# Optimization experiments

Hardware: AMD Instinct MI355X
Metric: run time of the kernel (lower is better)

Reference implementation:

```python
import jax, jax.numpy as jnp
import numpy as np

B, F, D, U = 4096, 32, 64, 256


def setup_inputs() -> dict:
    key = jax.random.key(0)
    k1, k2, k3, k4 = jax.random.split(key, 4)
    embeds = jax.random.normal(k1, (B, F, D), dtype=jnp.float32)
    # glorot-ish scaling for the learned weights
    linear_w = jax.random.normal(k2, (F * D, U), dtype=jnp.float32) * (2.0 / (F * D + U)) ** 0.5
    inner_w = jax.random.normal(k3, (U, F), dtype=jnp.float32) * (2.0 / (U + F)) ** 0.5
    outer_w = jax.random.normal(k4, (U, D, D), dtype=jnp.float32) * (2.0 / (2 * D)) ** 0.5
    return {"embeds": embeds, "linear_w": linear_w, "inner_w": inner_w, "outer_w": outer_w}


def reference(embeds, linear_w, inner_w, outer_w):
    b = embeds.shape[0]
    # linear signal lz: flatten fields and project -> [B, U]
    lz = embeds.reshape(b, -1) @ linear_w
    # inner products: per unit u, delta_u = sum_f w_{u,f} * e_f  -> [B, U, D];
    # lp_inner[b,u] = ||delta_u||^2 (collapses the per-unit TF loop into one einsum)
    delta = jnp.einsum('bfd,uf->bud', embeds, inner_w)
    lp_inner = jnp.sum(jnp.square(delta), axis=2)  # [B, U]
    # outer products: product = fs fs^T with fs = sum_f e_f; lp_outer[b,u] = <product_b, W_u>
    fs = jnp.sum(embeds, axis=1)  # [B, D]
    lp_outer = jnp.einsum('bi,bj,uij->bu', fs, fs, outer_w)  # [B, U]
    return jnp.concatenate([lz, lp_inner, lp_outer], axis=1)  # [B, 3U]
```

## Files before the change

kernel.cpp:

```cpp
#include <hip/hip_runtime.h>
#include <hip/hip_bf16.h>


#define KA 3072
#define KW 7168

typedef __attribute__((ext_vector_type(8))) short short8v;
typedef __attribute__((ext_vector_type(4))) float f32x4;

#define GLOAD(src, dst) __builtin_amdgcn_global_load_lds( \
    (const __attribute__((address_space(1))) void*)(src), \
    (__attribute__((address_space(3))) void*)(dst), 16, 0, 0)

static __device__ __forceinline__ short f2bf(float f) {
    union { float f; unsigned u; } v; v.f = f;
    unsigned r = v.u + 0x7fffu + ((v.u >> 16) & 1u);
    return (short)(r >> 16);
}
static __device__ __forceinline__ float bf2f(short s) {
    union { unsigned u; float f; } v; v.u = ((unsigned)(unsigned short)s) << 16;
    return v.f;
}
static __device__ __forceinline__ int cvtpk(float lo, float hi) {
    int r;
    asm("v_cvt_pk_bf16_f32 %0, %1, %2" : "=v"(r) : "v"(lo), "v"(hi));
    return r;
}

__global__ __launch_bounds__(256) void prep(const float* __restrict__ embeds,
                                            const float* __restrict__ lw,
                                            const float* __restrict__ iw,
                                            const float* __restrict__ ow,
                                            short* __restrict__ A,
                                            short* __restrict__ FS,
                                            short* __restrict__ Wt) {
    __shared__ float se[2048];
    __shared__ short sebf[2048];
    int t = threadIdx.x;

    if (blockIdx.x < 4096) {
        int b = blockIdx.x;
        const float* e = embeds + (size_t)b * 2048;
        short* arow = A + (size_t)b * KA;

        float4 v0 = ((const float4*)e)[t * 2];
        float4 v1 = ((const float4*)e)[t * 2 + 1];
        ((float4*)se)[t * 2] = v0;
        ((float4*)se)[t * 2 + 1] = v1;
        short8v sb;
        sb[0] = f2bf(v0.x); sb[1] = f2bf(v0.y); sb[2] = f2bf(v0.z); sb[3] = f2bf(v0.w);
        sb[4] = f2bf(v1.x); sb[5] = f2bf(v1.y); sb[6] = f2bf(v1.z); sb[7] = f2bf(v1.w);
        ((short8v*)sebf)[t] = sb;
        *(short8v*)&arow[t * 8] = sb;

        __syncthreads();
        if (t < 64) {
            float s = 0.f;
            #pragma unroll
            for (int f = 0; f < 32; ++f) s += se[f * 64 + t];
            FS[(size_t)b * 64 + t] = f2bf(s);
        }

        int wid = t >> 6, lane = t & 63;
        int tm = wid >> 1, tn = wid & 1;
        int lr = lane & 15, lk = (lane >> 4) * 8;
        f32x4 g = {0.f, 0.f, 0.f, 0.f};
        #pragma unroll
        for (int ks = 0; ks < 2; ++ks) {
            short8v a  = *(const short8v*)&sebf[(tm * 16 + lr) * 64 + ks * 32 + lk];
            short8v bb = *(const short8v*)&sebf[(tn * 16 + lr) * 64 + ks * 32 + lk];
            g = __builtin_amdgcn_mfma_f32_16x16x32_bf16(a, bb, g, 0, 0, 0);
        }
        #pragma unroll
        for (int r = 0; r < 4; ++r) {
            int grow = tm * 16 + (lane >> 4) * 4 + r;
            int gcol = tn * 16 + lr;
            arow[2048 + grow * 32 + gcol] = f2bf(g[r]);
        }
    } else {
        int u = blockIdx.x - 4096;
        short* w = Wt + (size_t)u * KW;

        for (int k = t; k < 2048; k += 256) w[k] = f2bf(lw[(size_t)k * 256 + u]);

        if (t < 32) se[t] = iw[u * 32 + t];
        __syncthreads();
        for (int idx = t; idx < 1024; idx += 256)
            w[2048 + idx] = f2bf(se[idx >> 5] * se[idx & 31]);

        const float* owu = ow + (size_t)u * 4096;
        for (int i = t; i < 512; i += 256) {
            float4 a = ((const float4*)owu)[i * 2];
            float4 b = ((const float4*)owu)[i * 2 + 1];
            short8v s;
            s[0] = f2bf(a.x); s[1] = f2bf(a.y); s[2] = f2bf(a.z); s[3] = f2bf(a.w);
            s[4] = f2bf(b.x); s[5] = f2bf(b.y); s[6] = f2bf(b.z); s[7] = f2bf(b.w);
            *(short8v*)&w[3072 + i * 8] = s;
        }
    }
}

__global__ __launch_bounds__(256) void gemm_tile(const short* __restrict__ A,
                                                 const short* __restrict__ Wt,
                                                 const short* __restrict__ FS,
                                                 float* __restrict__ out) {
    __shared__ short As[3][8192];
    __shared__ short Bs[3][4096];

    int id = blockIdx.x;
    int xcd = id & 7, slot = id >> 3, sgrp = slot >> 4, q = slot & 15;
    int seg = (sgrp == 0) ? 2 : (sgrp == 1) ? 0 : 1;
    int mt = xcd * 4 + (q >> 2), nt = q & 3;
    const int nk = (seg == 0) ? 32 : (seg == 1) ? 16 : 64;
    int brow = mt * 128, bcol = nt * 64;
    int akoff = (seg == 1) ? 2048 : 0;
    int boff  = (seg == 0) ? 0 : (seg == 1) ? 2048 : 3072;

    int t = threadIdx.x, w = t >> 6, lane = t & 63;
    int lr = lane & 15, hi = lane >> 4;
    int srow = t >> 3;
    int soct = (t & 7) ^ (srow & 7);

    const short* Asrc = A  + (size_t)(brow + srow) * KA + akoff + soct * 8;
    const short* Bsrc = Wt + (size_t)(bcol + srow) * KW + boff  + soct * 8;
    const short* Fsrc = FS + (size_t)(brow + srow) * 64 + soct * 8;

    auto stageA = [&](int p, int kt) {
        #pragma unroll
        for (int i = 0; i < 4; ++i)
            GLOAD(Asrc + (size_t)i * 32 * KA + kt * 64, &As[p][i * 2048 + t * 8]);
    };
    auto stageB = [&](int p, int kt) {
        #pragma unroll
        for (int i = 0; i < 2; ++i)
            GLOAD(Bsrc + (size_t)i * 32 * KW + kt * 64, &Bs[p][i * 2048 + t * 8]);
    };

    f32x4 acc[2][4];
    #pragma unroll
    for (int m = 0; m < 2; ++m)
        #pragma unroll
        for (int n = 0; n < 4; ++n) acc[m][n] = (f32x4){0.f, 0.f, 0.f, 0.f};

    auto compute = [&](const short* a_s, const short* b_s) {
        #pragma unroll
        for (int ks = 0; ks < 2; ++ks) {
            int oct = ((ks * 4 + hi) ^ (lr & 7)) * 8;
            short8v a[2], b[4];
            #pragma unroll
            for (int m = 0; m < 2; ++m)
                a[m] = *(const short8v*)&a_s[(w * 32 + m * 16 + lr) * 64 + oct];
            #pragma unroll
            for (int n = 0; n < 4; ++n)
                b[n] = *(const short8v*)&b_s[(n * 16 + lr) * 64 + oct];
            __builtin_amdgcn_s_setprio(1);
            #pragma unroll
            for (int m = 0; m < 2; ++m)
                #pragma unroll
                for (int n = 0; n < 4; ++n)
                    acc[m][n] = __builtin_amdgcn_mfma_f32_16x16x32_bf16(a[m], b[n], acc[m][n], 0, 0, 0);
            __builtin_amdgcn_s_setprio(0);
        }
    };

    if (seg != 2) {
        stageA(0, 0); stageB(0, 0);
        stageA(1, 1); stageB(1, 1);
        stageA(2, 2); stageB(2, 2);
        __builtin_amdgcn_sched_barrier(0);
        for (int kt = 0; kt < nk; ++kt) {
            int cur = kt % 3;
            if (kt + 2 < nk)      asm volatile("s_waitcnt vmcnt(12)" ::: "memory");
            else if (kt + 1 < nk) asm volatile("s_waitcnt vmcnt(6)" ::: "memory");
            else                  asm volatile("s_waitcnt vmcnt(0)" ::: "memory");
            __builtin_amdgcn_s_barrier();
            __builtin_amdgcn_sched_barrier(0);
            compute(As[cur], Bs[cur]);
            __builtin_amdgcn_sched_barrier(0);
            __builtin_amdgcn_s_barrier();
            if (kt + 3 < nk) { stageA(cur, kt + 3); stageB(cur, kt + 3); }
            __builtin_amdgcn_sched_barrier(0);
        }
    } else {
        #pragma unroll
        for (int i = 0; i < 4; ++i)
            GLOAD(Fsrc + (size_t)i * 32 * 64, &As[0][i * 2048 + t * 8]);
        stageB(0, 0); stageB(1, 1); stageB(2, 2);
        asm volatile("s_waitcnt vmcnt(6)" ::: "memory");
        __builtin_amdgcn_s_barrier();
        __builtin_amdgcn_sched_barrier(0);

        float fj[2][2][8];
        #pragma unroll
        for (int m = 0; m < 2; ++m)
            #pragma unroll
            for (int ks = 0; ks < 2; ++ks) {
                int oct = ((ks * 4 + hi) ^ (lr & 7)) * 8;
                short8v v = *(const short8v*)&As[0][(w * 32 + m * 16 + lr) * 64 + oct];
                #pragma unroll
                for (int e = 0; e < 8; ++e) fj[m][ks][e] = bf2f(v[e]);
            }
        for (int kt = 0; kt < 64; ++kt) {
            int cur = kt % 3;
            if (kt + 2 < 64)      asm volatile("s_waitcnt vmcnt(4)" ::: "memory");
            else if (kt + 1 < 64) asm volatile("s_waitcnt vmcnt(2)" ::: "memory");
            else                  asm volatile("s_waitcnt vmcnt(0)" ::: "memory");
            __builtin_amdgcn_s_barrier();
            __builtin_amdgcn_sched_barrier(0);
            int ioff = ((kt >> 3) ^ (lr & 7)) * 8 + (kt & 7);
            float s[2];
            #pragma unroll
            for (int m = 0; m < 2; ++m)
                s[m] = bf2f(As[0][(w * 32 + m * 16 + lr) * 64 + ioff]);
            #pragma unroll
            for (int ks = 0; ks < 2; ++ks) {
                int oct = ((ks * 4 + hi) ^ (lr & 7)) * 8;
                short8v b[4];
                #pragma unroll
                for (int n = 0; n < 4; ++n)
                    b[n] = *(const short8v*)&Bs[cur][(n * 16 + lr) * 64 + oct];
                #pragma unroll
                for (int m = 0; m < 2; ++m) {
                    union { int i32[4]; short8v v; } fa;
                    #pragma unroll
                    for (int q2 = 0; q2 < 4; ++q2)
                        fa.i32[q2] = cvtpk(s[m] * fj[m][ks][2 * q2], s[m] * fj[m][ks][2 * q2 + 1]);
                    __builtin_amdgcn_s_setprio(1);
                    #pragma unroll
                    for (int n = 0; n < 4; ++n)
                        acc[m][n] = __builtin_amdgcn_mfma_f32_16x16x32_bf16(fa.v, b[n], acc[m][n], 0, 0, 0);
                    __builtin_amdgcn_s_setprio(0);
                }
            }
            __builtin_amdgcn_sched_barrier(0);
            __builtin_amdgcn_s_barrier();
            if (kt + 3 < 64) stageB(cur, kt + 3);
            __builtin_amdgcn_sched_barrier(0);
        }
    }

    int segbase = seg * 256;
    #pragma unroll
    for (int m = 0; m < 2; ++m) {
        int row0 = brow + w * 32 + m * 16 + hi * 4;
        #pragma unroll
        for (int n = 0; n < 4; ++n) {
            int col = segbase + bcol + n * 16 + lr;
            #pragma unroll
            for (int r = 0; r < 4; ++r)
                out[(size_t)(row0 + r) * 768 + col] = acc[m][n][r];
        }
    }
}

extern "C" void kernel_launch(void* const* d_in, const int* in_sizes, int n_in,
                              void* d_out, int out_size, void* d_ws, size_t ws_size,
                              hipStream_t stream) {
    const float* embeds = (const float*)d_in[0];
    const float* lw = (const float*)d_in[1];
    const float* iw = (const float*)d_in[2];
    const float* ow = (const float*)d_in[3];
    float* out = (float*)d_out;

    short* A  = (short*)d_ws;
    short* Wt = A + (size_t)4096 * KA;
    short* FS = Wt + (size_t)256 * KW;

    prep<<<dim3(4352), dim3(256), 0, stream>>>(embeds, lw, iw, ow, A, FS, Wt);
    gemm_tile<<<dim3(384), dim3(256), 0, stream>>>(A, Wt, FS, out);
}
```

Baseline: 64.63 us.

## Split-K GEMM tiles into equal 16-step chunks with atomic accumulation

Work is split along K so every tile runs 16 k-steps: the linear segment is cut into 2 chunks and the outer segment into 4, and the grid grows from 384 to 896 blocks so the uneven per-segment load is balanced. Partial sums are combined with float atomic adds, so the prep kernel gets extra blocks that zero the output first. LDS pipelining drops from triple to double buffering, which frees shared memory and may raise occupancy. In exchange it adds atomic traffic, a zeroing pass, and a summation order that is no longer deterministic.

```diff
diff --git a/kernel.cpp b/kernel.cpp
--- a/kernel.cpp
+++ b/kernel.cpp
@@ -33,10 +33,19 @@
                                             const float* __restrict__ ow,
                                             short* __restrict__ A,
                                             short* __restrict__ FS,
-                                            short* __restrict__ Wt) {
+                                            short* __restrict__ Wt,
+                                            float4* __restrict__ outv) {
     __shared__ float se[2048];
     __shared__ short sebf[2048];
     int t = threadIdx.x;
+
+    if (blockIdx.x >= 4352) {
+        size_t i = (size_t)(blockIdx.x - 4352) * 256 + t;
+        #pragma unroll
+        for (int r = 0; r < 3; ++r)
+            outv[i + (size_t)r * 262144] = (float4){0.f, 0.f, 0.f, 0.f};
+        return;
+    }
 
     if (blockIdx.x < 4096) {
         int b = blockIdx.x;
@@ -104,17 +113,22 @@
                                                  const short* __restrict__ Wt,
                                                  const short* __restrict__ FS,
                                                  float* __restrict__ out) {
-    __shared__ short As[3][8192];
-    __shared__ short Bs[3][4096];
+    __shared__ short As[2][8192];
+    __shared__ short Bs[2][4096];
 
     int id = blockIdx.x;
-    int xcd = id & 7, slot = id >> 3, sgrp = slot >> 4, q = slot & 15;
-    int seg = (sgrp == 0) ? 2 : (sgrp == 1) ? 0 : 1;
-    int mt = xcd * 4 + (q >> 2), nt = q & 3;
-    const int nk = (seg == 0) ? 32 : (seg == 1) ? 16 : 64;
+    int xcd = id & 7, s = id >> 3;
+    int mtl = s & 3, part = s >> 2;
+    int ck = part >> 2, nt = part & 3;
+    int mt = xcd * 4 + mtl;
+    int seg, kc;
+    if (ck < 2)       { seg = 0; kc = ck; }
+    else if (ck == 2) { seg = 1; kc = 0; }
+    else              { seg = 2; kc = ck - 3; }
+    const int nk = 16;
     int brow = mt * 128, bcol = nt * 64;
-    int akoff = (seg == 1) ? 2048 : 0;
-    int boff  = (seg == 0) ? 0 : (seg == 1) ? 2048 : 3072;
+    int akoff = (seg == 0) ? kc * 1024 : 2048;
+    int boff  = (seg == 0) ? kc * 1024 : (seg == 1) ? 2048 : 3072 + kc * 1024;
 
     int t = threadIdx.x, w = t >> 6, lane = t & 63;
     int lr = lane & 15, hi = lane >> 4;
@@ -166,27 +180,25 @@
     if (seg != 2) {
         stageA(0, 0); stageB(0, 0);
         stageA(1, 1); stageB(1, 1);
-        stageA(2, 2); stageB(2, 2);
         __builtin_amdgcn_sched_barrier(0);
         for (int kt = 0; kt < nk; ++kt) {
-            int cur = kt % 3;
-            if (kt + 2 < nk)      asm volatile("s_waitcnt vmcnt(12)" ::: "memory");
-            else if (kt + 1 < nk) asm volatile("s_waitcnt vmcnt(6)" ::: "memory");
-            else                  asm volatile("s_waitcnt vmcnt(0)" ::: "memory");
+            int cur = kt & 1;
+            if (kt + 1 < nk) asm volatile("s_waitcnt vmcnt(6)" ::: "memory");
+            else             asm volatile("s_waitcnt vmcnt(0)" ::: "memory");
             __builtin_amdgcn_s_barrier();
             __builtin_amdgcn_sched_barrier(0);
             compute(As[cur], Bs[cur]);
             __builtin_amdgcn_sched_barrier(0);
             __builtin_amdgcn_s_barrier();
-            if (kt + 3 < nk) { stageA(cur, kt + 3); stageB(cur, kt + 3); }
+            if (kt + 2 < nk) { stageA(cur, kt + 2); stageB(cur, kt + 2); }
             __builtin_amdgcn_sched_barrier(0);
         }
     } else {
         #pragma unroll
         for (int i = 0; i < 4; ++i)
             GLOAD(Fsrc + (size_t)i * 32 * 64, &As[0][i * 2048 + t * 8]);
-        stageB(0, 0); stageB(1, 1); stageB(2, 2);
-        asm volatile("s_waitcnt vmcnt(6)" ::: "memory");
+        stageB(0, 0); stageB(1, 1);
+        asm volatile("s_waitcnt vmcnt(4)" ::: "memory");
         __builtin_amdgcn_s_barrier();
         __builtin_amdgcn_sched_barrier(0);
 
@@ -200,18 +212,18 @@
                 #pragma unroll
                 for (int e = 0; e < 8; ++e) fj[m][ks][e] = bf2f(v[e]);
             }
-        for (int kt = 0; kt < 64; ++kt) {
-            int cur = kt % 3;
-            if (kt + 2 < 64)      asm volatile("s_waitcnt vmcnt(4)" ::: "memory");
-            else if (kt + 1 < 64) asm volatile("s_waitcnt vmcnt(2)" ::: "memory");
-            else                  asm volatile("s_waitcnt vmcnt(0)" ::: "memory");
-            __builtin_amdgcn_s_barrier();
-            __builtin_amdgcn_sched_barrier(0);
-            int ioff = ((kt >> 3) ^ (lr & 7)) * 8 + (kt & 7);
-            float s[2];
+        for (int kt = 0; kt < nk; ++kt) {
+            int cur = kt & 1;
+            if (kt + 1 < nk) asm volatile("s_waitcnt vmcnt(2)" ::: "memory");
+            else             asm volatile("s_waitcnt vmcnt(0)" ::: "memory");
+            __builtin_amdgcn_s_barrier();
+            __builtin_amdgcn_sched_barrier(0);
+            int iidx = kc * 16 + kt;
+            int ioff = ((iidx >> 3) ^ (lr & 7)) * 8 + (iidx & 7);
+            float sv[2];
             #pragma unroll
             for (int m = 0; m < 2; ++m)
-                s[m] = bf2f(As[0][(w * 32 + m * 16 + lr) * 64 + ioff]);
+                sv[m] = bf2f(As[0][(w * 32 + m * 16 + lr) * 64 + ioff]);
             #pragma unroll
             for (int ks = 0; ks < 2; ++ks) {
                 int oct = ((ks * 4 + hi) ^ (lr & 7)) * 8;
@@ -224,7 +236,7 @@
                     union { int i32[4]; short8v v; } fa;
                     #pragma unroll
                     for (int q2 = 0; q2 < 4; ++q2)
-                        fa.i32[q2] = cvtpk(s[m] * fj[m][ks][2 * q2], s[m] * fj[m][ks][2 * q2 + 1]);
+                        fa.i32[q2] = cvtpk(sv[m] * fj[m][ks][2 * q2], sv[m] * fj[m][ks][2 * q2 + 1]);
                     __builtin_amdgcn_s_setprio(1);
                     #pragma unroll
                     for (int n = 0; n < 4; ++n)
@@ -234,7 +246,7 @@
             }
             __builtin_amdgcn_sched_barrier(0);
             __builtin_amdgcn_s_barrier();
-            if (kt + 3 < 64) stageB(cur, kt + 3);
+            if (kt + 2 < nk) stageB(cur, kt + 2);
             __builtin_amdgcn_sched_barrier(0);
         }
     }
@@ -248,7 +260,7 @@
             int col = segbase + bcol + n * 16 + lr;
             #pragma unroll
             for (int r = 0; r < 4; ++r)
-                out[(size_t)(row0 + r) * 768 + col] = acc[m][n][r];
+                unsafeAtomicAdd(&out[(size_t)(row0 + r) * 768 + col], acc[m][n][r]);
         }
     }
 }
@@ -266,6 +278,6 @@
     short* Wt = A + (size_t)4096 * KA;
     short* FS = Wt + (size_t)256 * KW;
 
-    prep<<<dim3(4352), dim3(256), 0, stream>>>(embeds, lw, iw, ow, A, FS, Wt);
-    gemm_tile<<<dim3(384), dim3(256), 0, stream>>>(A, Wt, FS, out);
-}
+    prep<<<dim3(5376), dim3(256), 0, stream>>>(embeds, lw, iw, ow, A, FS, Wt, (float4*)out);
+    gemm_tile<<<dim3(896), dim3(256), 0, stream>>>(A, Wt, FS, out);
+}
```

Measured after the change: 62.67 us. -3.0%, faster.
